# Kernel tuning notes

Measured on AMD Instinct MI355X. Metric: run time of the kernel, lower is better.

## Reference

```python
import jax, jax.numpy as jnp
import numpy as np
import math

B, E, H, HD, P, G, N, L, FF = 16, 768, 12, 64, 16, 14, 196, 12, 3072
SQRT_E = math.sqrt(E)
SQRT_HD = math.sqrt(HD)


def cosine_norm(x):
    n = jnp.linalg.norm(x, axis=-1, keepdims=True)
    return x / jnp.maximum(n, 1e-6)


def layer_norm(x, w, b, eps=1e-6):
    m = jnp.mean(x, axis=-1, keepdims=True)
    v = jnp.var(x, axis=-1, keepdims=True)
    return (x - m) / jnp.sqrt(v + eps) * w + b


def setup_inputs() -> dict:
    key = jax.random.key(0)
    ks = jax.random.split(key, 16)
    std = 0.02
    return {
        "x": jax.random.normal(ks[0], (B, 3, 224, 224), jnp.float32),
        "patch_w": jax.random.normal(ks[1], (E, 3, P, P), jnp.float32) * std,
        "patch_b": jnp.zeros((E,), jnp.float32),
        "cls_token": jax.random.normal(ks[2], (1, 1, E), jnp.float32) * std,
        "pos_embed": jax.random.normal(ks[3], (1, N + 1, E), jnp.float32) * std,
        "Wq": jax.random.normal(ks[4], (L, E, E), jnp.float32) * std,
        "Wk": jax.random.normal(ks[5], (L, E, E), jnp.float32) * std,
        "Wv": jax.random.normal(ks[6], (L, E, E), jnp.float32) * std,
        "Wo": jax.random.normal(ks[7], (L, E, E), jnp.float32) * std,
        # Scale params stored at their torch init values (s = ones * scale)
        "s_qk": jnp.ones((L, H, HD), jnp.float32) / SQRT_E,        # scale=1/sqrt(dim)
        "Wup": jax.random.normal(ks[8], (L, FF, E), jnp.float32) * std,
        "Wgate": jax.random.normal(ks[9], (L, FF, E), jnp.float32) * std,
        "Wdown": jax.random.normal(ks[10], (L, E, FF), jnp.float32) * std,
        "s_u": jnp.ones((L, FF), jnp.float32),
        "s_v": jnp.ones((L, FF), jnp.float32),
        "alpha_A": jnp.ones((L, E), jnp.float32) / SQRT_E,         # scale=1/sqrt(dim)
        "alpha_M": jnp.ones((L, E), jnp.float32) / SQRT_E,
        "fc_w": jnp.ones((E,), jnp.float32),
        "fc_b": jnp.zeros((E,), jnp.float32),
    }


def _attention(h, wq, wk, wv, wo, s_qk):
    b, n, _ = h.shape
    q = (h @ wq.T).reshape(b, n, H, HD)
    k = (h @ wk.T).reshape(b, n, H, HD)
    v = (h @ wv.T).reshape(b, n, H, HD)
    # Scale.forward(): s * (init/scale) with init=1, scale=1/sqrt(E)
    s = s_qk * SQRT_E                                   # [H, HD]
    q = cosine_norm(q) * s
    k = cosine_norm(k) * s
    logits = jnp.einsum("bnhd,bmhd->bhnm", q, k) * SQRT_HD
    attn = jax.nn.softmax(logits, axis=-1)
    out = jnp.einsum("bhnm,bmhd->bnhd", attn, v).reshape(b, n, E)
    return out @ wo.T


def _mlp(h, wup, wgate, wdown, s_u, s_v):
    u = (h @ wup.T) * s_u
    v = (h @ wgate.T) * s_v * SQRT_E                    # mlp scale = sqrt(in_features)
    hidden = u * jax.nn.silu(v)
    return hidden @ wdown.T


def _block(h, wq, wk, wv, wo, s_qk, wup, wgate, wdown, s_u, s_v, a_A, a_M):
    # alpha Scale: init=0.05, scale=1/sqrt(E) -> effective = s * 0.05 * sqrt(E)
    aA = a_A * (0.05 * SQRT_E)
    aM = a_M * (0.05 * SQRT_E)
    h_A = cosine_norm(_attention(h, wq, wk, wv, wo, s_qk))
    h = cosine_norm(h + aA * (h_A - h))
    h_M = cosine_norm(_mlp(h, wup, wgate, wdown, s_u, s_v))
    h = cosine_norm(h + aM * (h_M - h))
    return h


def reference(x, patch_w, patch_b, cls_token, pos_embed, Wq, Wk, Wv, Wo, s_qk,
              Wup, Wgate, Wdown, s_u, s_v, alpha_A, alpha_M, fc_w, fc_b):
    b = x.shape[0]
    # patch embed: conv k=stride=16 == patch extraction + linear proj
    patches = x.reshape(b, 3, G, P, G, P).transpose(0, 2, 4, 1, 3, 5).reshape(b, N, 3 * P * P)
    t = patches @ patch_w.reshape(E, -1).T + patch_b    # [B, N, E]
    t = jnp.concatenate([jnp.broadcast_to(cls_token, (b, 1, E)), t], axis=1)
    t = t + pos_embed                                    # [B, N+1, E]
    nodes = None
    for i in range(L):
        t = _block(t, Wq[i], Wk[i], Wv[i], Wo[i], s_qk[i],
                   Wup[i], Wgate[i], Wdown[i], s_u[i], s_v[i], alpha_A[i], alpha_M[i])
        if i == L - 2:
            nodes = layer_norm(t, fc_w, fc_b)[:, 1:]
    edges = layer_norm(t, fc_w, fc_b)[:, 1:]
    return nodes, edges
```

## Files before the change

kernel.cpp:

```cpp
#include <hip/hip_runtime.h>
#include <hip/hip_bf16.h>
#include <cstdint>
#include <cstddef>

typedef __hip_bfloat16 bf16;
typedef short bf16x8 __attribute__((ext_vector_type(8)));
typedef float f32x4 __attribute__((ext_vector_type(4)));

#define SQRT_E   27.712812921102035f
#define ASCALE   (0.05f * 27.712812921102035f)
#define MPAD     3200

__device__ __forceinline__ void load_lds16(const bf16* g, bf16* l) {
    __builtin_amdgcn_global_load_lds(
        (const __attribute__((address_space(1))) void*)g,
        (__attribute__((address_space(3))) void*)l, 16, 0, 0);
}

__device__ __forceinline__ float block_sum(float v, float* sbuf) {
#pragma unroll
    for (int m = 32; m >= 1; m >>= 1) v += __shfl_xor(v, m);
    __syncthreads();
    if ((threadIdx.x & 63) == 0) sbuf[threadIdx.x >> 6] = v;
    __syncthreads();
    return sbuf[0] + sbuf[1] + sbuf[2] + sbuf[3];
}

__device__ __forceinline__ void cvt8(const float* s, bf16* d) {
    float4 f0 = *(const float4*)s;
    float4 f1 = *(const float4*)(s + 4);
    bf16 t[8];
    t[0] = __float2bfloat16(f0.x); t[1] = __float2bfloat16(f0.y);
    t[2] = __float2bfloat16(f0.z); t[3] = __float2bfloat16(f0.w);
    t[4] = __float2bfloat16(f1.x); t[5] = __float2bfloat16(f1.y);
    t[6] = __float2bfloat16(f1.z); t[7] = __float2bfloat16(f1.w);
    *reinterpret_cast<uint4*>(d) = *reinterpret_cast<const uint4*>(t);
}

__global__ __launch_bounds__(256) void conv1_kernel(const float* __restrict__ src,
                                                    bf16* __restrict__ dst, int n8) {
    int idx = blockIdx.x * 256 + threadIdx.x;
    if (idx >= n8) return;
    cvt8(src + (size_t)idx * 8, dst + (size_t)idx * 8);
}

__global__ __launch_bounds__(256) void wconv_kernel(
    const float* __restrict__ wq, const float* __restrict__ wk,
    const float* __restrict__ wv, const float* __restrict__ wo,
    const float* __restrict__ wu, const float* __restrict__ wg,
    const float* __restrict__ wd, bf16* __restrict__ dst) {
    int idx = blockIdx.x * 256 + threadIdx.x;
    if (idx >= 1179648) return;
    const float* src;
    size_t off;
    if (idx < 294912) {
        int seg = idx / 73728, o = idx - seg * 73728;
        src = (seg == 0) ? wq : (seg == 1) ? wk : (seg == 2) ? wv : wo;
        off = (size_t)o * 8;
    } else {
        int i2 = idx - 294912;
        int seg = i2 / 294912, o = i2 - seg * 294912;
        src = (seg == 0) ? wu : (seg == 1) ? wg : wd;
        off = (size_t)o * 8;
    }
    cvt8(src + off, dst + (size_t)idx * 8);
}

__global__ __launch_bounds__(256) void im2col_kernel(const float* __restrict__ x,
                                                     bf16* __restrict__ A) {
    int idx = blockIdx.x * 256 + threadIdx.x;
    int row = idx / 768, col = idx - row * 768;
    if (row >= 3136) { A[idx] = __float2bfloat16(0.f); return; }
    int b = row / 196, pp = row - b * 196;
    int gy = pp / 14, gx = pp - gy * 14;
    int c = col >> 8, rem = col & 255, py = rem >> 4, px = rem & 15;
    A[idx] = __float2bfloat16(
        x[((size_t)(b * 3 + c) * 224 + gy * 16 + py) * 224 + gx * 16 + px]);
}

__global__ __launch_bounds__(256) void assemble_kernel(
    const float* __restrict__ tproj, const float* __restrict__ pb,
    const float* __restrict__ cls, const float* __restrict__ pos,
    float* __restrict__ h, bf16* __restrict__ hb) {
    int row = blockIdx.x;
    int b = row / 197, n = row - b * 197;
#pragma unroll
    for (int i = 0; i < 3; i++) {
        int c = threadIdx.x + i * 256;
        float v;
        if (n == 0) v = cls[c] + pos[c];
        else v = tproj[(size_t)(b * 196 + n - 1) * 768 + c] + pb[c] + pos[(size_t)n * 768 + c];
        h[(size_t)row * 768 + c] = v;
        hb[(size_t)row * 768 + c] = __float2bfloat16(v);
    }
}

__global__ __launch_bounds__(256) void gemm_bt(
    const bf16* __restrict__ A, int lda,
    const bf16* __restrict__ B0, const bf16* __restrict__ B1, const bf16* __restrict__ B2,
    int tilesPerSeg, int segColStride,
    void* __restrict__ Cv, int ldc, long long partStride,
    int Klen, int ldb, int outBf16) {
    __shared__ __align__(16) bf16 As[128 * 32];
    __shared__ __align__(16) bf16 Bs[128 * 32];
    const int tid = threadIdx.x;
    const int lane = tid & 63, wave = tid >> 6;
    const int wm = wave & 1, wn = wave >> 1;
    const int quad = lane >> 4, l16 = lane & 15;
    const int seg = blockIdx.x / tilesPerSeg;
    const int nt = blockIdx.x - seg * tilesPerSeg;
    const bf16* B = (seg == 0) ? B0 : (seg == 1 ? B1 : B2);
    const int row0 = blockIdx.y * 128;
    const int col0 = nt * 128;
    const long long kofs = (long long)blockIdx.z * Klen;
    const bf16* Ab = A + (size_t)row0 * lda + kofs;
    const bf16* Bb = B + (size_t)col0 * ldb + kofs;
    const long long cofs = (long long)blockIdx.z * partStride + (long long)seg * segColStride;

    f32x4 acc[4][4];
    f32x4 zero = {0.f, 0.f, 0.f, 0.f};
#pragma unroll
    for (int i = 0; i < 4; i++)
#pragma unroll
        for (int j = 0; j < 4; j++) acc[i][j] = zero;

    for (int k0 = 0; k0 < Klen; k0 += 32) {
#pragma unroll
        for (int it = 0; it < 2; ++it) {
            int cidx = it * 256 + tid;
            int r = cidx >> 2, cg = cidx & 3;
            load_lds16(Ab + (size_t)r * lda + k0 + cg * 8, As + cidx * 8);
            load_lds16(Bb + (size_t)r * ldb + k0 + cg * 8, Bs + cidx * 8);
        }
        __syncthreads();
        bf16x8 av[4], bv[4];
#pragma unroll
        for (int i = 0; i < 4; i++) {
            av[i] = *(const bf16x8*)(As + (wm * 64 + i * 16 + l16) * 32 + quad * 8);
            bv[i] = *(const bf16x8*)(Bs + (wn * 64 + i * 16 + l16) * 32 + quad * 8);
        }
#pragma unroll
        for (int i = 0; i < 4; i++)
#pragma unroll
            for (int j = 0; j < 4; j++)
                acc[i][j] = __builtin_amdgcn_mfma_f32_16x16x32_bf16(av[i], bv[j], acc[i][j], 0, 0, 0);
        __syncthreads();
    }
    if (outBf16) {
        bf16* Cb = (bf16*)Cv + cofs;
#pragma unroll
        for (int i = 0; i < 4; i++) {
            int rr = row0 + wm * 64 + i * 16 + quad * 4;
#pragma unroll
            for (int j = 0; j < 4; j++) {
                int cc = col0 + wn * 64 + j * 16 + l16;
#pragma unroll
                for (int r = 0; r < 4; r++)
                    Cb[(size_t)(rr + r) * ldc + cc] = __float2bfloat16(acc[i][j][r]);
            }
        }
    } else {
        float* Cb = (float*)Cv + cofs;
#pragma unroll
        for (int i = 0; i < 4; i++) {
            int rr = row0 + wm * 64 + i * 16 + quad * 4;
#pragma unroll
            for (int j = 0; j < 4; j++) {
                int cc = col0 + wn * 64 + j * 16 + l16;
#pragma unroll
                for (int r = 0; r < 4; r++)
                    Cb[(size_t)(rr + r) * ldc + cc] = acc[i][j][r];
            }
        }
    }
}

__global__ __launch_bounds__(256) void gemm_qkv(
    const bf16* __restrict__ A,
    const bf16* __restrict__ Bq, const bf16* __restrict__ Bk, const bf16* __restrict__ Bv,
    const float* __restrict__ s_l,
    bf16* __restrict__ Qd, bf16* __restrict__ Kd, bf16* __restrict__ VTd) {
    __shared__ __align__(16) bf16 As[128 * 32];
    __shared__ __align__(16) bf16 Bs[128 * 32];
    const int tid = threadIdx.x;
    const int lane = tid & 63, wave = tid >> 6;
    const int wm = wave & 1, wn = wave >> 1;
    const int quad = lane >> 4, l16 = lane & 15;
    const int seg = blockIdx.x / 6;
    const int nt = blockIdx.x - seg * 6;
    const bf16* B = (seg == 0) ? Bq : (seg == 1 ? Bk : Bv);
    const int row0 = blockIdx.y * 128;
    const int col0 = nt * 128;
    const bf16* Ab = A + (size_t)row0 * 768;
    const bf16* Bb = B + (size_t)col0 * 768;

    f32x4 acc[4][4];
    f32x4 zero = {0.f, 0.f, 0.f, 0.f};
#pragma unroll
    for (int i = 0; i < 4; i++)
#pragma unroll
        for (int j = 0; j < 4; j++) acc[i][j] = zero;

    for (int k0 = 0; k0 < 768; k0 += 32) {
#pragma unroll
        for (int it = 0; it < 2; ++it) {
            int cidx = it * 256 + tid;
            int r = cidx >> 2, cg = cidx & 3;
            load_lds16(Ab + (size_t)r * 768 + k0 + cg * 8, As + cidx * 8);
            load_lds16(Bb + (size_t)r * 768 + k0 + cg * 8, Bs + cidx * 8);
        }
        __syncthreads();
        bf16x8 av[4], bv[4];
#pragma unroll
        for (int i = 0; i < 4; i++) {
            av[i] = *(const bf16x8*)(As + (wm * 64 + i * 16 + l16) * 32 + quad * 8);
            bv[i] = *(const bf16x8*)(Bs + (wn * 64 + i * 16 + l16) * 32 + quad * 8);
        }
#pragma unroll
        for (int i = 0; i < 4; i++)
#pragma unroll
            for (int j = 0; j < 4; j++)
                acc[i][j] = __builtin_amdgcn_mfma_f32_16x16x32_bf16(av[i], bv[j], acc[i][j], 0, 0, 0);
        __syncthreads();
    }

    const int hcol = nt * 2 + wn;
    if (seg < 2) {
        bf16* Dst = (seg == 0) ? Qd : Kd;
        float sv0[4];
#pragma unroll
        for (int j = 0; j < 4; j++) sv0[j] = s_l[hcol * 64 + j * 16 + l16] * SQRT_E;
#pragma unroll
        for (int i = 0; i < 4; i++) {
#pragma unroll
            for (int r = 0; r < 4; r++) {
                float ss = acc[i][0][r] * acc[i][0][r] + acc[i][1][r] * acc[i][1][r]
                         + acc[i][2][r] * acc[i][2][r] + acc[i][3][r] * acc[i][3][r];
#pragma unroll
                for (int m = 1; m < 16; m <<= 1) ss += __shfl_xor(ss, m);
                float inv = 1.f / fmaxf(sqrtf(ss), 1e-6f);
                int t = row0 + wm * 64 + i * 16 + quad * 4 + r;
                if (t < 3152) {
                    int b = t / 197, n = t - b * 197;
                    size_t base = ((size_t)(b * 12 + hcol) * 208 + n) * 64;
#pragma unroll
                    for (int j = 0; j < 4; j++)
                        Dst[base + j * 16 + l16] =
                            __float2bfloat16(acc[i][j][r] * inv * sv0[j]);
                }
            }
        }
    } else {
#pragma unroll
        for (int i = 0; i < 4; i++) {
#pragma unroll
            for (int r = 0; r < 4; r++) {
                int t = row0 + wm * 64 + i * 16 + quad * 4 + r;
                if (t < 3152) {
                    int b = t / 197, n = t - b * 197;
                    size_t vbase = (size_t)(b * 12 + hcol) * 64 * 224 + n;
#pragma unroll
                    for (int j = 0; j < 4; j++)
                        VTd[vbase + (size_t)(j * 16 + l16) * 224] =
                            __float2bfloat16(acc[i][j][r]);
                }
            }
        }
    }
}

__global__ __launch_bounds__(256) void gemm_upgate(
    const bf16* __restrict__ A, const bf16* __restrict__ Bu, const bf16* __restrict__ Bv,
    const float* __restrict__ su, const float* __restrict__ sv,
    bf16* __restrict__ H) {
    __shared__ __align__(16) bf16 As[128 * 32];
    __shared__ __align__(16) bf16 Bus[64 * 32];
    __shared__ __align__(16) bf16 Bvs[64 * 32];
    const int tid = threadIdx.x;
    const int lane = tid & 63, wave = tid >> 6;
    const int wm = wave & 1, wn = wave >> 1;
    const int quad = lane >> 4, l16 = lane & 15;
    const int ct = blockIdx.x;
    const int row0 = blockIdx.y * 128;
    const bf16* Ab = A + (size_t)row0 * 768;
    const bf16* Bub = Bu + (size_t)ct * 64 * 768;
    const bf16* Bvb = Bv + (size_t)ct * 64 * 768;

    f32x4 au[4][2], av_[4][2];
    f32x4 zero = {0.f, 0.f, 0.f, 0.f};
#pragma unroll
    for (int i = 0; i < 4; i++)
#pragma unroll
        for (int j = 0; j < 2; j++) { au[i][j] = zero; av_[i][j] = zero; }

    for (int k0 = 0; k0 < 768; k0 += 32) {
#pragma unroll
        for (int it = 0; it < 2; ++it) {
            int cidx = it * 256 + tid;
            int r = cidx >> 2, cg = cidx & 3;
            load_lds16(Ab + (size_t)r * 768 + k0 + cg * 8, As + cidx * 8);
        }
        {
            int r = tid >> 2, cg = tid & 3;
            load_lds16(Bub + (size_t)r * 768 + k0 + cg * 8, Bus + tid * 8);
            load_lds16(Bvb + (size_t)r * 768 + k0 + cg * 8, Bvs + tid * 8);
        }
        __syncthreads();
        bf16x8 a[4], bu[2], bv[2];
#pragma unroll
        for (int i = 0; i < 4; i++)
            a[i] = *(const bf16x8*)(As + (wm * 64 + i * 16 + l16) * 32 + quad * 8);
#pragma unroll
        for (int j = 0; j < 2; j++) {
            bu[j] = *(const bf16x8*)(Bus + (wn * 32 + j * 16 + l16) * 32 + quad * 8);
            bv[j] = *(const bf16x8*)(Bvs + (wn * 32 + j * 16 + l16) * 32 + quad * 8);
        }
#pragma unroll
        for (int i = 0; i < 4; i++)
#pragma unroll
            for (int j = 0; j < 2; j++) {
                au[i][j]  = __builtin_amdgcn_mfma_f32_16x16x32_bf16(a[i], bu[j], au[i][j], 0, 0, 0);
                av_[i][j] = __builtin_amdgcn_mfma_f32_16x16x32_bf16(a[i], bv[j], av_[i][j], 0, 0, 0);
            }
        __syncthreads();
    }
#pragma unroll
    for (int j = 0; j < 2; j++) {
        int cc = ct * 64 + wn * 32 + j * 16 + l16;
        float suc = su[cc];
        float svc = sv[cc] * SQRT_E;
#pragma unroll
        for (int i = 0; i < 4; i++) {
            int rr = row0 + wm * 64 + i * 16 + quad * 4;
#pragma unroll
            for (int r = 0; r < 4; r++) {
                float u = au[i][j][r] * suc;
                float v = av_[i][j][r] * svc;
                float sig = 1.f / (1.f + __expf(-v));
                H[(size_t)(rr + r) * 3072 + cc] = __float2bfloat16(u * v * sig);
            }
        }
    }
}

__global__ __launch_bounds__(64) void attn_kernel(
    const bf16* __restrict__ Q, const bf16* __restrict__ K,
    const bf16* __restrict__ VT, bf16* __restrict__ O) {
    __shared__ __align__(16) bf16 Ps[16 * 224];
    int lane = threadIdx.x;
    int quad = lane >> 4, l16 = lane & 15;
    int bh = blockIdx.x % 192;
    int qt = blockIdx.x / 192;
    int b = bh / 12, h = bh - b * 12;
    const bf16* Qb = Q + (size_t)bh * 208 * 64;
    const bf16* Kb = K + (size_t)bh * 208 * 64;
    const bf16* Vb = VT + (size_t)bh * 64 * 224;
    f32x4 zero = {0.f, 0.f, 0.f, 0.f};

    bf16x8 a0 = *(const bf16x8*)(Qb + (qt * 16 + l16) * 64 + quad * 8);
    bf16x8 a1 = *(const bf16x8*)(Qb + (qt * 16 + l16) * 64 + quad * 8 + 32);

    f32x4 lg[13];
#pragma unroll
    for (int kt = 0; kt < 13; kt++) {
        bf16x8 b0 = *(const bf16x8*)(Kb + (kt * 16 + l16) * 64 + quad * 8);
        bf16x8 b1 = *(const bf16x8*)(Kb + (kt * 16 + l16) * 64 + quad * 8 + 32);
        f32x4 c = zero;
        c = __builtin_amdgcn_mfma_f32_16x16x32_bf16(a0, b0, c, 0, 0, 0);
        c = __builtin_amdgcn_mfma_f32_16x16x32_bf16(a1, b1, c, 0, 0, 0);
        lg[kt] = c;
    }
    float mx[4] = {-3e38f, -3e38f, -3e38f, -3e38f};
#pragma unroll
    for (int kt = 0; kt < 13; kt++) {
        bool valid = (kt * 16 + l16) < 197;
#pragma unroll
        for (int r = 0; r < 4; r++) {
            float v = valid ? lg[kt][r] * 8.0f : -3e38f;
            lg[kt][r] = v;
            mx[r] = fmaxf(mx[r], v);
        }
    }
#pragma unroll
    for (int m = 1; m < 16; m <<= 1)
#pragma unroll
        for (int r = 0; r < 4; r++) mx[r] = fmaxf(mx[r], __shfl_xor(mx[r], m));
    float sm[4] = {0.f, 0.f, 0.f, 0.f};
#pragma unroll
    for (int kt = 0; kt < 13; kt++)
#pragma unroll
        for (int r = 0; r < 4; r++) {
            float p = __expf(lg[kt][r] - mx[r]);
            lg[kt][r] = p;
            sm[r] += p;
        }
#pragma unroll
    for (int m = 1; m < 16; m <<= 1)
#pragma unroll
        for (int r = 0; r < 4; r++) sm[r] += __shfl_xor(sm[r], m);
    float inv[4];
#pragma unroll
    for (int r = 0; r < 4; r++) inv[r] = 1.f / sm[r];
#pragma unroll
    for (int kt = 0; kt < 13; kt++)
#pragma unroll
        for (int r = 0; r < 4; r++)
            Ps[(quad * 4 + r) * 224 + kt * 16 + l16] = __float2bfloat16(lg[kt][r] * inv[r]);
#pragma unroll
    for (int r = 0; r < 4; r++)
        Ps[(quad * 4 + r) * 224 + 208 + l16] = __float2bfloat16(0.f);
    __syncthreads();
#pragma unroll
    for (int nt = 0; nt < 4; nt++) {
        f32x4 o = zero;
#pragma unroll
        for (int ks = 0; ks < 7; ks++) {
            bf16x8 pa = *(const bf16x8*)(Ps + l16 * 224 + ks * 32 + quad * 8);
            bf16x8 vb = *(const bf16x8*)(Vb + (nt * 16 + l16) * 224 + ks * 32 + quad * 8);
            o = __builtin_amdgcn_mfma_f32_16x16x32_bf16(pa, vb, o, 0, 0, 0);
        }
#pragma unroll
        for (int r = 0; r < 4; r++) {
            int tok = qt * 16 + quad * 4 + r;
            if (tok < 197)
                O[(size_t)(b * 197 + tok) * 768 + h * 64 + nt * 16 + l16] = __float2bfloat16(o[r]);
        }
    }
}

__global__ __launch_bounds__(256) void residual_cos(
    const float* __restrict__ proj, int nParts, long long partStride,
    const float* __restrict__ alpha,
    float* __restrict__ h, bf16* __restrict__ hb) {
    __shared__ float sbuf[4];
    int row = blockIdx.x, tid = threadIdx.x;
    float p[3];
    float ss = 0.f;
#pragma unroll
    for (int i = 0; i < 3; i++) {
        int c = tid + i * 256;
        float v = 0.f;
        for (int pt = 0; pt < nParts; pt++) v += proj[(long long)pt * partStride + (size_t)row * 768 + c];
        p[i] = v;
        ss += v * v;
    }
    ss = block_sum(ss, sbuf);
    float inv1 = 1.f / fmaxf(sqrtf(ss), 1e-6f);
    float ss2 = 0.f;
#pragma unroll
    for (int i = 0; i < 3; i++) {
        int c = tid + i * 256;
        float hv = h[(size_t)row * 768 + c];
        float a = alpha[c] * ASCALE;
        float m = hv + a * (p[i] * inv1 - hv);
        p[i] = m;
        ss2 += m * m;
    }
    ss2 = block_sum(ss2, sbuf);
    float inv2 = 1.f / fmaxf(sqrtf(ss2), 1e-6f);
#pragma unroll
    for (int i = 0; i < 3; i++) {
        int c = tid + i * 256;
        float v = p[i] * inv2;
        h[(size_t)row * 768 + c] = v;
        hb[(size_t)row * 768 + c] = __float2bfloat16(v);
    }
}

__global__ __launch_bounds__(256) void layernorm_out(
    const float* __restrict__ h, const float* __restrict__ w,
    const float* __restrict__ bia, float* __restrict__ out) {
    __shared__ float sbuf[4];
    int bi = blockIdx.x;
    int b = bi / 196, j = bi - b * 196;
    int row = b * 197 + j + 1;
    int tid = threadIdx.x;
    float xv[3];
    float s = 0.f;
#pragma unroll
    for (int i = 0; i < 3; i++) {
        xv[i] = h[(size_t)row * 768 + tid + i * 256];
        s += xv[i];
    }
    s = block_sum(s, sbuf);
    float mean = s * (1.f / 768.f);
    float s2 = 0.f;
#pragma unroll
    for (int i = 0; i < 3; i++) { float d = xv[i] - mean; s2 += d * d; }
    s2 = block_sum(s2, sbuf);
    float var = s2 * (1.f / 768.f);
    float invs = 1.f / sqrtf(var + 1e-6f);
#pragma unroll
    for (int i = 0; i < 3; i++) {
        int c = tid + i * 256;
        out[(size_t)bi * 768 + c] = (xv[i] - mean) * invs * w[c] + bia[c];
    }
}

extern "C" void kernel_launch(void* const* d_in, const int* in_sizes, int n_in,
                              void* d_out, int out_size, void* d_ws, size_t ws_size,
                              hipStream_t stream) {
    (void)in_sizes; (void)n_in; (void)out_size; (void)ws_size;
    const float* x      = (const float*)d_in[0];
    const float* patchw = (const float*)d_in[1];
    const float* patchb = (const float*)d_in[2];
    const float* cls    = (const float*)d_in[3];
    const float* pos    = (const float*)d_in[4];
    const float* Wq     = (const float*)d_in[5];
    const float* Wk     = (const float*)d_in[6];
    const float* Wv     = (const float*)d_in[7];
    const float* Wo     = (const float*)d_in[8];
    const float* s_qk   = (const float*)d_in[9];
    const float* Wup    = (const float*)d_in[10];
    const float* Wgate  = (const float*)d_in[11];
    const float* Wdown  = (const float*)d_in[12];
    const float* s_u    = (const float*)d_in[13];
    const float* s_v    = (const float*)d_in[14];
    const float* alA    = (const float*)d_in[15];
    const float* alM    = (const float*)d_in[16];
    const float* fcw    = (const float*)d_in[17];
    const float* fcb    = (const float*)d_in[18];
    float* out = (float*)d_out;

    char* ws = (char*)d_ws;
    size_t ofs = 0;
    auto alloc = [&](size_t bytes) -> void* {
        void* p = ws + ofs;
        ofs += (bytes + 255) & ~(size_t)255;
        return p;
    };
    float* h      = (float*)alloc((size_t)MPAD * 768 * 4);
    float* part   = (float*)alloc((size_t)4 * MPAD * 768 * 4);
    bf16*  hb     = (bf16*)alloc((size_t)MPAD * 768 * 2);
    bf16*  attno  = (bf16*)alloc((size_t)MPAD * 768 * 2);
    bf16*  hidden = (bf16*)alloc((size_t)MPAD * 3072 * 2);
    size_t qkvt_bytes = ((size_t)192 * 208 * 64 * 2) * 2 + (size_t)192 * 64 * 224 * 2;
    bf16*  Qb     = (bf16*)alloc(qkvt_bytes);
    bf16*  Kb     = Qb + (size_t)192 * 208 * 64;
    bf16*  VTb    = Kb + (size_t)192 * 208 * 64;
    bf16*  wbf    = (bf16*)alloc((size_t)9437184 * 2);

    float* tproj  = part;
    bf16*  Apatch = hidden;

    bf16* wqb = wbf;
    bf16* wkb = wbf + 589824;
    bf16* wvb = wbf + 1179648;
    bf16* wob = wbf + 1769472;
    bf16* wub = wbf + 2359296;
    bf16* wgb = wbf + 4718592;
    bf16* wdb = wbf + 7077888;

    const long long PSTR = (long long)MPAD * 768;
    const size_t EE = 768 * 768, FE = (size_t)3072 * 768;

    conv1_kernel<<<288, 256, 0, stream>>>(patchw, wqb, 73728);
    im2col_kernel<<<9600, 256, 0, stream>>>(x, Apatch);
    gemm_bt<<<dim3(6, 25, 1), 256, 0, stream>>>(Apatch, 768, wqb, wqb, wqb,
                                                6, 0, tproj, 768, 0, 768, 768, 0);
    assemble_kernel<<<3152, 256, 0, stream>>>(tproj, patchb, cls, pos, h, hb);
    hipMemsetAsync(Qb, 0, qkvt_bytes, stream);

    for (int l = 0; l < 12; l++) {
        wconv_kernel<<<4608, 256, 0, stream>>>(Wq + (size_t)l * EE, Wk + (size_t)l * EE,
                                               Wv + (size_t)l * EE, Wo + (size_t)l * EE,
                                               Wup + (size_t)l * FE, Wgate + (size_t)l * FE,
                                               Wdown + (size_t)l * FE, wbf);
        gemm_qkv<<<dim3(18, 25), 256, 0, stream>>>(hb, wqb, wkb, wvb,
                                                   s_qk + (size_t)l * 768, Qb, Kb, VTb);
        attn_kernel<<<2496, 64, 0, stream>>>(Qb, Kb, VTb, attno);
        gemm_bt<<<dim3(6, 25, 2), 256, 0, stream>>>(attno, 768, wob, wob, wob,
                                                    6, 0, part, 768, PSTR, 384, 768, 0);
        residual_cos<<<3152, 256, 0, stream>>>(part, 2, PSTR, alA + (size_t)l * 768, h, hb);
        gemm_upgate<<<dim3(48, 25), 256, 0, stream>>>(hb, wub, wgb,
                                                      s_u + (size_t)l * 3072,
                                                      s_v + (size_t)l * 3072, hidden);
        gemm_bt<<<dim3(6, 25, 4), 256, 0, stream>>>(hidden, 3072, wdb, wdb, wdb,
                                                    6, 0, part, 768, PSTR, 768, 3072, 0);
        residual_cos<<<3152, 256, 0, stream>>>(part, 4, PSTR, alM + (size_t)l * 768, h, hb);

        if (l == 10) layernorm_out<<<3136, 256, 0, stream>>>(h, fcw, fcb, out);
        if (l == 11) layernorm_out<<<3136, 256, 0, stream>>>(h, fcw, fcb, out + 2408448);
    }
}
```

Measured before the change: 2.505 ms.

## Overlap next-layer weight conversion with output projection via double-buffered weights

Merges the patch-weight conversion, im2col and layer-0 weight conversion into one prep launch. The per-layer fp32-to-bf16 weight conversion is folded into the output-projection GEMM launch as extra blocks that convert the next layer's weights into a second buffer. The small 300-block o-proj GEMM then shares the GPU with conversion work instead of running as separate serialized launches. This adds a second weight buffer and creates contention between the GEMM and the bandwidth-bound conversion blocks.

```diff
diff --git a/kernel.cpp b/kernel.cpp
--- a/kernel.cpp
+++ b/kernel.cpp
@@ -37,20 +37,12 @@
     *reinterpret_cast<uint4*>(d) = *reinterpret_cast<const uint4*>(t);
 }
 
-__global__ __launch_bounds__(256) void conv1_kernel(const float* __restrict__ src,
-                                                    bf16* __restrict__ dst, int n8) {
-    int idx = blockIdx.x * 256 + threadIdx.x;
-    if (idx >= n8) return;
-    cvt8(src + (size_t)idx * 8, dst + (size_t)idx * 8);
-}
-
-__global__ __launch_bounds__(256) void wconv_kernel(
+__device__ __forceinline__ void wconv_body(
+    int idx,
     const float* __restrict__ wq, const float* __restrict__ wk,
     const float* __restrict__ wv, const float* __restrict__ wo,
     const float* __restrict__ wu, const float* __restrict__ wg,
     const float* __restrict__ wd, bf16* __restrict__ dst) {
-    int idx = blockIdx.x * 256 + threadIdx.x;
-    if (idx >= 1179648) return;
     const float* src;
     size_t off;
     if (idx < 294912) {
@@ -66,16 +58,30 @@
     cvt8(src + off, dst + (size_t)idx * 8);
 }
 
-__global__ __launch_bounds__(256) void im2col_kernel(const float* __restrict__ x,
-                                                     bf16* __restrict__ A) {
-    int idx = blockIdx.x * 256 + threadIdx.x;
-    int row = idx / 768, col = idx - row * 768;
-    if (row >= 3136) { A[idx] = __float2bfloat16(0.f); return; }
-    int b = row / 196, pp = row - b * 196;
-    int gy = pp / 14, gx = pp - gy * 14;
-    int c = col >> 8, rem = col & 255, py = rem >> 4, px = rem & 15;
-    A[idx] = __float2bfloat16(
-        x[((size_t)(b * 3 + c) * 224 + gy * 16 + py) * 224 + gx * 16 + px]);
+__global__ __launch_bounds__(256) void prep_kernel(
+    const float* __restrict__ x, bf16* __restrict__ A,
+    const float* __restrict__ patchw, bf16* __restrict__ pwb,
+    const float* __restrict__ wq, const float* __restrict__ wk,
+    const float* __restrict__ wv, const float* __restrict__ wo,
+    const float* __restrict__ wu, const float* __restrict__ wg,
+    const float* __restrict__ wd, bf16* __restrict__ wdst) {
+    int b = blockIdx.x, tid = threadIdx.x;
+    if (b < 288) {
+        int idx = b * 256 + tid;
+        cvt8(patchw + (size_t)idx * 8, pwb + (size_t)idx * 8);
+    } else if (b < 9888) {
+        int idx = (b - 288) * 256 + tid;
+        int row = idx / 768, col = idx - row * 768;
+        if (row >= 3136) { A[idx] = __float2bfloat16(0.f); return; }
+        int bb = row / 196, pp = row - bb * 196;
+        int gy = pp / 14, gx = pp - gy * 14;
+        int c = col >> 8, rem = col & 255, py = rem >> 4, px = rem & 15;
+        A[idx] = __float2bfloat16(
+            x[((size_t)(bb * 3 + c) * 224 + gy * 16 + py) * 224 + gx * 16 + px]);
+    } else {
+        int idx = (b - 9888) * 256 + tid;
+        wconv_body(idx, wq, wk, wv, wo, wu, wg, wd, wdst);
+    }
 }
 
 __global__ __launch_bounds__(256) void assemble_kernel(
@@ -171,6 +177,75 @@
                 for (int r = 0; r < 4; r++)
                     Cb[(size_t)(rr + r) * ldc + cc] = acc[i][j][r];
             }
+        }
+    }
+}
+
+__global__ __launch_bounds__(256) void oproj_wconv(
+    const bf16* __restrict__ A, const bf16* __restrict__ Bw,
+    float* __restrict__ C, long long partStride,
+    const float* __restrict__ wq, const float* __restrict__ wk,
+    const float* __restrict__ wv, const float* __restrict__ wo,
+    const float* __restrict__ wu, const float* __restrict__ wg,
+    const float* __restrict__ wd, bf16* __restrict__ wdst) {
+    __shared__ __align__(16) bf16 As[128 * 32];
+    __shared__ __align__(16) bf16 Bs[128 * 32];
+    const int bb = blockIdx.x;
+    const int tid = threadIdx.x;
+    if (bb >= 300) {
+        int idx = (bb - 300) * 256 + tid;
+        wconv_body(idx, wq, wk, wv, wo, wu, wg, wd, wdst);
+        return;
+    }
+    const int lane = tid & 63, wave = tid >> 6;
+    const int wm = wave & 1, wn = wave >> 1;
+    const int quad = lane >> 4, l16 = lane & 15;
+    const int nt = bb % 6;
+    const int ry = (bb / 6) % 25;
+    const int z  = bb / 150;
+    const int row0 = ry * 128, col0 = nt * 128;
+    const bf16* Ab = A + (size_t)row0 * 768 + z * 384;
+    const bf16* Bb = Bw + (size_t)col0 * 768 + z * 384;
+
+    f32x4 acc[4][4];
+    f32x4 zero = {0.f, 0.f, 0.f, 0.f};
+#pragma unroll
+    for (int i = 0; i < 4; i++)
+#pragma unroll
+        for (int j = 0; j < 4; j++) acc[i][j] = zero;
+
+    for (int k0 = 0; k0 < 384; k0 += 32) {
+#pragma unroll
+        for (int it = 0; it < 2; ++it) {
+            int cidx = it * 256 + tid;
+            int r = cidx >> 2, cg = cidx & 3;
+            load_lds16(Ab + (size_t)r * 768 + k0 + cg * 8, As + cidx * 8);
+            load_lds16(Bb + (size_t)r * 768 + k0 + cg * 8, Bs + cidx * 8);
+        }
+        __syncthreads();
+        bf16x8 av[4], bv[4];
+#pragma unroll
+        for (int i = 0; i < 4; i++) {
+            av[i] = *(const bf16x8*)(As + (wm * 64 + i * 16 + l16) * 32 + quad * 8);
+            bv[i] = *(const bf16x8*)(Bs + (wn * 64 + i * 16 + l16) * 32 + quad * 8);
+        }
+#pragma unroll
+        for (int i = 0; i < 4; i++)
+#pragma unroll
+            for (int j = 0; j < 4; j++)
+                acc[i][j] = __builtin_amdgcn_mfma_f32_16x16x32_bf16(av[i], bv[j], acc[i][j], 0, 0, 0);
+        __syncthreads();
+    }
+    float* Cb = C + (long long)z * partStride;
+#pragma unroll
+    for (int i = 0; i < 4; i++) {
+        int rr = row0 + wm * 64 + i * 16 + quad * 4;
+#pragma unroll
+        for (int j = 0; j < 4; j++) {
+            int cc = col0 + wn * 64 + j * 16 + l16;
+#pragma unroll
+            for (int r = 0; r < 4; r++)
+                Cb[(size_t)(rr + r) * 768 + cc] = acc[i][j][r];
         }
     }
 }
@@ -538,39 +613,45 @@
     bf16*  Qb     = (bf16*)alloc(qkvt_bytes);
     bf16*  Kb     = Qb + (size_t)192 * 208 * 64;
     bf16*  VTb    = Kb + (size_t)192 * 208 * 64;
-    bf16*  wbf    = (bf16*)alloc((size_t)9437184 * 2);
+    const size_t WPL = 9437184;
+    bf16*  wbf0   = (bf16*)alloc(WPL * 2);
+    bf16*  wbf1   = (bf16*)alloc(WPL * 2);
+    bf16*  pwb    = (bf16*)alloc((size_t)589824 * 2);
 
     float* tproj  = part;
     bf16*  Apatch = hidden;
 
-    bf16* wqb = wbf;
-    bf16* wkb = wbf + 589824;
-    bf16* wvb = wbf + 1179648;
-    bf16* wob = wbf + 1769472;
-    bf16* wub = wbf + 2359296;
-    bf16* wgb = wbf + 4718592;
-    bf16* wdb = wbf + 7077888;
-
     const long long PSTR = (long long)MPAD * 768;
     const size_t EE = 768 * 768, FE = (size_t)3072 * 768;
 
-    conv1_kernel<<<288, 256, 0, stream>>>(patchw, wqb, 73728);
-    im2col_kernel<<<9600, 256, 0, stream>>>(x, Apatch);
-    gemm_bt<<<dim3(6, 25, 1), 256, 0, stream>>>(Apatch, 768, wqb, wqb, wqb,
+    prep_kernel<<<14496, 256, 0, stream>>>(x, Apatch, patchw, pwb,
+                                           Wq, Wk, Wv, Wo, Wup, Wgate, Wdown, wbf0);
+    gemm_bt<<<dim3(6, 25, 1), 256, 0, stream>>>(Apatch, 768, pwb, pwb, pwb,
                                                 6, 0, tproj, 768, 0, 768, 768, 0);
     assemble_kernel<<<3152, 256, 0, stream>>>(tproj, patchb, cls, pos, h, hb);
     hipMemsetAsync(Qb, 0, qkvt_bytes, stream);
 
     for (int l = 0; l < 12; l++) {
-        wconv_kernel<<<4608, 256, 0, stream>>>(Wq + (size_t)l * EE, Wk + (size_t)l * EE,
-                                               Wv + (size_t)l * EE, Wo + (size_t)l * EE,
-                                               Wup + (size_t)l * FE, Wgate + (size_t)l * FE,
-                                               Wdown + (size_t)l * FE, wbf);
+        bf16* wl    = (l & 1) ? wbf1 : wbf0;
+        bf16* wnext = (l & 1) ? wbf0 : wbf1;
+        bf16* wqb = wl;
+        bf16* wkb = wl + 589824;
+        bf16* wvb = wl + 1179648;
+        bf16* wob = wl + 1769472;
+        bf16* wub = wl + 2359296;
+        bf16* wgb = wl + 4718592;
+        bf16* wdb = wl + 7077888;
+        int ln = (l < 11) ? (l + 1) : l;
+
         gemm_qkv<<<dim3(18, 25), 256, 0, stream>>>(hb, wqb, wkb, wvb,
                                                    s_qk + (size_t)l * 768, Qb, Kb, VTb);
         attn_kernel<<<2496, 64, 0, stream>>>(Qb, Kb, VTb, attno);
-        gemm_bt<<<dim3(6, 25, 2), 256, 0, stream>>>(attno, 768, wob, wob, wob,
-                                                    6, 0, part, 768, PSTR, 384, 768, 0);
+        oproj_wconv<<<(l < 11) ? 4908 : 300, 256, 0, stream>>>(
+            attno, wob, part, PSTR,
+            Wq + (size_t)ln * EE, Wk + (size_t)ln * EE,
+            Wv + (size_t)ln * EE, Wo + (size_t)ln * EE,
+            Wup + (size_t)ln * FE, Wgate + (size_t)ln * FE,
+            Wdown + (size_t)ln * FE, wnext);
         residual_cos<<<3152, 256, 0, stream>>>(part, 2, PSTR, alA + (size_t)l * 768, h, hb);
         gemm_upgate<<<dim3(48, 25), 256, 0, stream>>>(hb, wub, wgb,
                                                       s_u + (size_t)l * 3072,
```

Result: faster. 2.434 ms (-2.8%).
